# Kernel tuning notes

Hardware: AMD Instinct MI355X
Metric: run time of the kernel (lower is better)

The kernel has to match this reference:

```python
import jax, jax.numpy as jnp
import numpy as np

N = 2_000_000
NUM_IN = 9
F1, F2 = 32, 64
NUM_SEG = 100_000
EPS = 1e-5


def setup_inputs() -> dict:
    key = jax.random.key(0)
    ks = jax.random.split(key, 10)
    points = jax.random.normal(ks[0], (N, NUM_IN), dtype=jnp.float32)
    inverse_indices = jax.random.randint(ks[1], (N,), 0, NUM_SEG, dtype=jnp.int64)
    w1 = jax.random.normal(ks[2], (NUM_IN, F1), dtype=jnp.float32) / np.sqrt(NUM_IN)
    b1 = jax.random.normal(ks[3], (F1,), dtype=jnp.float32) * 0.01
    g1 = jnp.ones((F1,), jnp.float32)
    be1 = jnp.zeros((F1,), jnp.float32)
    w2 = jax.random.normal(ks[4], (F1, F2), dtype=jnp.float32) / np.sqrt(F1)
    b2 = jax.random.normal(ks[5], (F2,), dtype=jnp.float32) * 0.01
    g2 = jnp.ones((F2,), jnp.float32)
    be2 = jnp.zeros((F2,), jnp.float32)
    return {
        "points": points, "inverse_indices": inverse_indices, "num_segments": NUM_SEG,
        "w1": w1, "b1": b1, "g1": g1, "be1": be1,
        "w2": w2, "b2": b2, "g2": g2, "be2": be2,
    }


def _linear_bn_relu(x, w, b, gamma, beta):
    # Linear -> BatchNorm1d (training-mode batch stats, biased var, eps=1e-5) -> ReLU
    h = x @ w + b
    mean = h.mean(axis=0)
    var = h.var(axis=0)  # biased, matches torch BN normalization
    h = (h - mean) * jax.lax.rsqrt(var + EPS) * gamma + beta
    return jax.nn.relu(h)


def reference(points, inverse_indices, num_segments, w1, b1, g1, be1, w2, b2, g2, be2):
    feat = _linear_bn_relu(points, w1, b1, g1, be1)
    feat = _linear_bn_relu(feat, w2, b2, g2, be2)
    # scatter_max over dim 0; torch_scatter zero-initializes empty segments,
    # and post-ReLU features are >= 0, so clamp -inf (empty) to 0.
    seg = jax.ops.segment_max(feat, inverse_indices, num_segments=num_segments)
    return jnp.maximum(seg, 0.0)
```

## Files before the change

kernel.cpp:

```cpp
#include <hip/hip_runtime.h>

#define EPS 1e-5f
#define NIN 9
#define F1 32
#define F2 64
#define NMOM 45
#define ROWB 80
#define SHIFT 7
#define NSEGB 128
#define NBMAX 1024
#define BT_BIN 8192
#define WSTRIDE 68

#define WS_S    0
#define WS_M    16
#define WS_S2   64
#define WS_SS2  128
#define WS_SC1  192
#define WS_SH1  224
#define WS_W1P  256
#define WS_SC2  544
#define WS_SH2  608

typedef __attribute__((ext_vector_type(8))) short bf16x8;
typedef __attribute__((ext_vector_type(4))) float f32x4;

__device__ __forceinline__ unsigned int f2bf(float f) {
    unsigned int u = __float_as_uint(f);
    return (u + 0x7fffu + ((u >> 16) & 1u)) >> 16;
}
__device__ __forceinline__ unsigned int pack2(float lo, float hi) {
    return f2bf(lo) | (f2bf(hi) << 16);
}

__global__ __launch_bounds__(256, 4) void moments_kernel(
    const float* __restrict__ pts, const int* __restrict__ idx,
    float* __restrict__ ws, int* __restrict__ histc, int N, int nb)
{
    __shared__ int lhist[NBMAX];
    __shared__ float red[64];
    for (int t = threadIdx.x; t < nb; t += 256) lhist[t] = 0;

    float S[NIN], M[NMOM];
#pragma unroll
    for (int k = 0; k < NIN; ++k) S[k] = 0.f;
#pragma unroll
    for (int m = 0; m < NMOM; ++m) M[m] = 0.f;
    __syncthreads();

    const int stride = gridDim.x * blockDim.x;
    for (int i = blockIdx.x * blockDim.x + threadIdx.x; i < N; i += stride) {
        const float* p = pts + (size_t)i * NIN;
        atomicAdd(&lhist[idx[i] >> SHIFT], 1);
        float x[NIN];
#pragma unroll
        for (int k = 0; k < NIN; ++k) x[k] = p[k];
#pragma unroll
        for (int k = 0; k < NIN; ++k) {
            S[k] += x[k];
#pragma unroll
            for (int l = 0; l < NIN; ++l) {
                if (l >= k) {
                    const int m = k * NIN - (k * (k - 1)) / 2 + (l - k);
                    M[m] = fmaf(x[k], x[l], M[m]);
                }
            }
        }
    }
#pragma unroll
    for (int off = 32; off > 0; off >>= 1) {
#pragma unroll
        for (int k = 0; k < NIN; ++k) S[k] += __shfl_xor(S[k], off, 64);
#pragma unroll
        for (int m = 0; m < NMOM; ++m) M[m] += __shfl_xor(M[m], off, 64);
    }
    if (threadIdx.x < 64) red[threadIdx.x] = 0.f;
    __syncthreads();
    if ((threadIdx.x & 63) == 0) {
#pragma unroll
        for (int k = 0; k < NIN; ++k) atomicAdd(&red[WS_S + k], S[k]);
#pragma unroll
        for (int m = 0; m < NMOM; ++m) atomicAdd(&red[WS_M + m], M[m]);
    }
    __syncthreads();
    if (threadIdx.x < 64) atomicAdd(&ws[threadIdx.x], red[threadIdx.x]);
    for (int t = threadIdx.x; t < nb; t += 256)
        if (lhist[t] > 0) atomicAdd(&histc[t], lhist[t]);
}

__global__ void scan_coarse_kernel(const int* __restrict__ histc,
                                   int* __restrict__ offsets,
                                   int* __restrict__ cursor, int nb)
{
    __shared__ int part[256];
    const int tid = threadIdx.x;
    int v[4];
    int sum = 0;
    const int base = tid * 4;
#pragma unroll
    for (int j = 0; j < 4; ++j) {
        const int i = base + j;
        v[j] = (i < nb) ? histc[i] : 0;
        sum += v[j];
    }
    part[tid] = sum;
    __syncthreads();
    for (int d = 1; d < 256; d <<= 1) {
        int t = (tid >= d) ? part[tid - d] : 0;
        __syncthreads();
        part[tid] += t;
        __syncthreads();
    }
    int pre = part[tid] - sum;
#pragma unroll
    for (int j = 0; j < 4; ++j) {
        const int i = base + j;
        if (i < nb) { offsets[i] = pre; cursor[i] = pre; }
        pre += v[j];
    }
    if (tid == 255) offsets[nb] = part[255];
}

__global__ void finalize1_kernel(
    const float* __restrict__ w1, const float* __restrict__ b1,
    const float* __restrict__ g1, const float* __restrict__ be1,
    float* __restrict__ ws, float invN)
{
    __shared__ float sc1s[F1];
    const int j = threadIdx.x;
    if (j < F1) {
        float W[NIN];
        float P = 0.f;
#pragma unroll
        for (int k = 0; k < NIN; ++k) {
            W[k] = w1[k * F1 + j];
            P = fmaf(ws[WS_S + k], W[k], P);
        }
        float Q = 0.f;
        int m = 0;
#pragma unroll
        for (int k = 0; k < NIN; ++k) {
            Q = fmaf(ws[WS_M + m], W[k] * W[k], Q); ++m;
#pragma unroll
            for (int l = k + 1; l < NIN; ++l) {
                Q = fmaf(2.f * ws[WS_M + m], W[k] * W[l], Q); ++m;
            }
        }
        const float b = b1[j];
        const float mean = fmaf(P, invN, b);
        const float Eh2 = fmaf(fmaf(2.f * b, P, Q), invN, b * b);
        const float var = Eh2 - mean * mean;
        const float sc = g1[j] * rsqrtf(var + EPS);
        ws[WS_SC1 + j] = sc;
        ws[WS_SH1 + j] = be1[j] - mean * sc;
        sc1s[j] = sc;
    }
    __syncthreads();
    for (int m = threadIdx.x; m < NIN * F1; m += blockDim.x)
        ws[WS_W1P + m] = w1[m] * sc1s[m & (F1 - 1)];
}

__global__ void finalize2_kernel(
    const float* __restrict__ g2, const float* __restrict__ be2,
    const float* __restrict__ b2, float* __restrict__ ws, float invN, float padf)
{
    const int j = threadIdx.x;
    if (j < F2) {
        const float b = b2[j];
        const float S  = ws[WS_S2 + j]  - padf * b;
        const float SS = ws[WS_SS2 + j] - padf * b * b;
        const float mean = S * invN;
        const float var  = SS * invN - mean * mean;
        const float sc   = g2[j] * rsqrtf(var + EPS);
        ws[WS_SC2 + j] = sc;
        ws[WS_SH2 + j] = be2[j] - mean * sc;
    }
}

__device__ __forceinline__ void f1_row_bf16(
    const float* __restrict__ p, const float* __restrict__ wl,
    const float* __restrict__ sh1, unsigned int* __restrict__ pk )
{
    float x[NIN];
#pragma unroll
    for (int k = 0; k < NIN; ++k) x[k] = p[k];
#pragma unroll
    for (int fc = 0; fc < 4; ++fc) {
        float h[8];
#pragma unroll
        for (int jj = 0; jj < 8; ++jj) h[jj] = sh1[fc * 8 + jj];
#pragma unroll
        for (int k = 0; k < NIN; ++k) {
            const float xv = x[k];
#pragma unroll
            for (int jj = 0; jj < 8; ++jj)
                h[jj] = fmaf(xv, wl[k * F1 + fc * 8 + jj], h[jj]);
        }
#pragma unroll
        for (int jj = 0; jj < 4; ++jj)
            pk[fc * 4 + jj] = pack2(fmaxf(h[2 * jj], 0.f), fmaxf(h[2 * jj + 1], 0.f));
    }
}

__global__ __launch_bounds__(256, 3) void f1stats_kernel(
    const float* __restrict__ pts, const float* __restrict__ w2,
    const float* __restrict__ b2, float* __restrict__ ws,
    uint4* __restrict__ f1buf, int N)
{
    __shared__ __align__(16) unsigned char stag[4][64 * ROWB];
    __shared__ float red[2 * F2];

    const int lane = threadIdx.x & 63, wv = threadIdx.x >> 6;
    const int quad = lane >> 4, m16 = lane & 15;

    bf16x8 bfr[4];
#pragma unroll
    for (int nt = 0; nt < 4; ++nt)
#pragma unroll
        for (int j = 0; j < 8; ++j)
            bfr[nt][j] = (short)f2bf(w2[(quad * 8 + j) * F2 + nt * 16 + m16]);
    float b2f[4];
#pragma unroll
    for (int nt = 0; nt < 4; ++nt) b2f[nt] = b2[nt * 16 + m16];

    const float* wl  = ws + WS_W1P;
    const float* sh1 = ws + WS_SH1;
    const f32x4 zero = {0.f, 0.f, 0.f, 0.f};
    float s[4] = {0.f, 0.f, 0.f, 0.f}, ss[4] = {0.f, 0.f, 0.f, 0.f};

    unsigned char* myst = stag[wv];
    const int nchunks = (N + 63) / 64;
    for (int c = blockIdx.x * 4 + wv; c < nchunks; c += gridDim.x * 4) {
        const int i = c * 64 + lane;
        unsigned int pk[16];
        if (i < N) {
            f1_row_bf16(pts + (size_t)i * NIN, wl, sh1, pk);
        } else {
#pragma unroll
            for (int q = 0; q < 16; ++q) pk[q] = 0u;
        }
        uint4* wrow = (uint4*)(myst + lane * ROWB);
#pragma unroll
        for (int cidx = 0; cidx < 4; ++cidx)
            wrow[cidx] = make_uint4(pk[4*cidx+0], pk[4*cidx+1], pk[4*cidx+2], pk[4*cidx+3]);

        if (i < N) {
            uint4* dst = f1buf + (size_t)i * 4;
            dst[0] = make_uint4(pk[0],  pk[1],  pk[2],  pk[3]);
            dst[1] = make_uint4(pk[4],  pk[5],  pk[6],  pk[7]);
            dst[2] = make_uint4(pk[8],  pk[9],  pk[10], pk[11]);
            dst[3] = make_uint4(pk[12], pk[13], pk[14], pk[15]);
        }

        bf16x8 afr[4];
#pragma unroll
        for (int mt = 0; mt < 4; ++mt)
            afr[mt] = *(const bf16x8*)(myst + (mt * 16 + m16) * ROWB + quad * 16);
#pragma unroll
        for (int mt = 0; mt < 4; ++mt) {
#pragma unroll
            for (int nt = 0; nt < 4; ++nt) {
                f32x4 d = __builtin_amdgcn_mfma_f32_16x16x32_bf16(afr[mt], bfr[nt], zero, 0, 0, 0);
#pragma unroll
                for (int rr = 0; rr < 4; ++rr) {
                    const float v = d[rr] + b2f[nt];
                    s[nt] += v;
                    ss[nt] = fmaf(v, v, ss[nt]);
                }
            }
        }
    }

#pragma unroll
    for (int off = 16; off < 64; off <<= 1)
#pragma unroll
        for (int nt = 0; nt < 4; ++nt) {
            s[nt]  += __shfl_xor(s[nt], off, 64);
            ss[nt] += __shfl_xor(ss[nt], off, 64);
        }
    if (threadIdx.x < 2 * F2) red[threadIdx.x] = 0.f;
    __syncthreads();
    if (quad == 0) {
#pragma unroll
        for (int nt = 0; nt < 4; ++nt) {
            atomicAdd(&red[nt * 16 + m16], s[nt]);
            atomicAdd(&red[F2 + nt * 16 + m16], ss[nt]);
        }
    }
    __syncthreads();
    if (threadIdx.x < F2) {
        atomicAdd(&ws[WS_S2 + threadIdx.x],  red[threadIdx.x]);
        atomicAdd(&ws[WS_SS2 + threadIdx.x], red[F2 + threadIdx.x]);
    }
}

__global__ __launch_bounds__(256) void binning_kernel(
    const int* __restrict__ idx, int* __restrict__ cursor,
    int2* __restrict__ pair, int N, int nb)
{
    __shared__ int lcnt[NBMAX];
    __shared__ int runbase[NBMAX];
    const int tid = threadIdx.x;
    const int t0 = blockIdx.x * BT_BIN;
    for (int t = tid; t < nb; t += 256) lcnt[t] = 0;
    __syncthreads();
#pragma unroll 4
    for (int r = 0; r < BT_BIN / 256; ++r) {
        const int i = t0 + r * 256 + tid;
        if (i < N) atomicAdd(&lcnt[idx[i] >> SHIFT], 1);
    }
    __syncthreads();
    for (int t = tid; t < nb; t += 256) {
        const int c = lcnt[t];
        if (c > 0) runbase[t] = atomicAdd(&cursor[t], c);
        lcnt[t] = 0;
    }
    __syncthreads();
#pragma unroll 4
    for (int r = 0; r < BT_BIN / 256; ++r) {
        const int i = t0 + r * 256 + tid;
        if (i < N) {
            const int sg = idx[i];
            const int bb = sg >> SHIFT;
            const int p = runbase[bb] + atomicAdd(&lcnt[bb], 1);
            pair[p] = make_int2(i, sg);
        }
    }
}

__global__ __launch_bounds__(256, 3) void bucket_scatter_kernel(
    const uint4* __restrict__ f1buf, const int2* __restrict__ pair,
    const float* __restrict__ w2, const float* __restrict__ b2,
    const float* __restrict__ ws, const int* __restrict__ offsets,
    unsigned int* __restrict__ out, int nseg)
{
    __shared__ unsigned int win[NSEGB * WSTRIDE];
    __shared__ int2 prl[4][64];

    const int b = blockIdx.x;
    const int start = offsets[b], end = offsets[b + 1];
    const int tid = threadIdx.x;
    const int lane = tid & 63, wv = tid >> 6;
    const int quad = lane >> 4, m16 = lane & 15;

    for (int t = tid; t < NSEGB * WSTRIDE; t += 256) win[t] = 0u;

    bf16x8 bfr[4];
#pragma unroll
    for (int nt = 0; nt < 4; ++nt)
#pragma unroll
        for (int j = 0; j < 8; ++j)
            bfr[nt][j] = (short)f2bf(w2[(quad * 8 + j) * F2 + nt * 16 + m16]);
    float sc2f[4], shb[4];
#pragma unroll
    for (int nt = 0; nt < 4; ++nt) {
        const int f = nt * 16 + m16;
        sc2f[nt] = ws[WS_SC2 + f];
        shb[nt]  = fmaf(b2[f], sc2f[nt], ws[WS_SH2 + f]);
    }
    const f32x4 zero = {0.f, 0.f, 0.f, 0.f};
    __syncthreads();

    const int segbase = b << SHIFT;
    const int nch = (end - start + 63) >> 6;
    const bf16x8* fb = (const bf16x8*)f1buf;
    for (int c = wv; c < nch; c += 4) {
        const int cbase = start + c * 64;
        const int sp = cbase + lane;
        int2 pr = make_int2(0, -1);
        if (sp < end) {
            pr = pair[sp];
            pr.y -= segbase;
        }
        prl[wv][lane] = pr;

        bf16x8 afr[4];
#pragma unroll
        for (int mt = 0; mt < 4; ++mt) {
            if (cbase + mt * 16 + m16 < end) {
                const int gi = prl[wv][mt * 16 + m16].x;
                afr[mt] = fb[(size_t)gi * 4 + quad];
            } else {
#pragma unroll
                for (int j = 0; j < 8; ++j) afr[mt][j] = 0;
            }
        }
#pragma unroll
        for (int mt = 0; mt < 4; ++mt) {
            f32x4 d[4];
#pragma unroll
            for (int nt = 0; nt < 4; ++nt)
                d[nt] = __builtin_amdgcn_mfma_f32_16x16x32_bf16(afr[mt], bfr[nt], zero, 0, 0, 0);
#pragma unroll
            for (int rr = 0; rr < 4; ++rr) {
                const int sl = prl[wv][mt * 16 + quad * 4 + rr].y;
                if (sl >= 0) {
#pragma unroll
                    for (int nt = 0; nt < 4; ++nt) {
                        const float v = fmaf(d[nt][rr], sc2f[nt], shb[nt]);
                        if (v > 0.f)
                            atomicMax(&win[sl * WSTRIDE + nt * 16 + m16], __float_as_uint(v));
                    }
                }
            }
        }
    }
    __syncthreads();
    const int rows = min(NSEGB, nseg - segbase);
    for (int t = tid; t < rows * 64; t += 256)
        out[(size_t)(segbase + (t >> 6)) * 64 + (t & 63)] = win[(t >> 6) * WSTRIDE + (t & 63)];
}

__global__ __launch_bounds__(256, 3) void stats2_kernel(
    const float* __restrict__ pts, const float* __restrict__ w2,
    const float* __restrict__ b2, float* __restrict__ ws, int N)
{
    __shared__ __align__(16) unsigned char stag[4][64 * ROWB];
    __shared__ float red[2 * F2];

    const int lane = threadIdx.x & 63, wv = threadIdx.x >> 6;
    const int quad = lane >> 4, m16 = lane & 15;

    bf16x8 bfr[4];
#pragma unroll
    for (int nt = 0; nt < 4; ++nt)
#pragma unroll
        for (int j = 0; j < 8; ++j)
            bfr[nt][j] = (short)f2bf(w2[(quad * 8 + j) * F2 + nt * 16 + m16]);
    float b2f[4];
#pragma unroll
    for (int nt = 0; nt < 4; ++nt) b2f[nt] = b2[nt * 16 + m16];

    const float* wl  = ws + WS_W1P;
    const float* sh1 = ws + WS_SH1;
    const f32x4 zero = {0.f, 0.f, 0.f, 0.f};
    float s[4] = {0.f, 0.f, 0.f, 0.f}, ss[4] = {0.f, 0.f, 0.f, 0.f};

    unsigned char* myst = stag[wv];
    const int nchunks = (N + 63) / 64;
    for (int c = blockIdx.x * 4 + wv; c < nchunks; c += gridDim.x * 4) {
        const int i = c * 64 + lane;
        unsigned int pk[16];
        if (i < N) {
            f1_row_bf16(pts + (size_t)i * NIN, wl, sh1, pk);
        } else {
#pragma unroll
            for (int q = 0; q < 16; ++q) pk[q] = 0u;
        }
        uint4* wrow = (uint4*)(myst + lane * ROWB);
#pragma unroll
        for (int cidx = 0; cidx < 4; ++cidx)
            wrow[cidx] = make_uint4(pk[4*cidx+0], pk[4*cidx+1], pk[4*cidx+2], pk[4*cidx+3]);

        bf16x8 afr[4];
#pragma unroll
        for (int mt = 0; mt < 4; ++mt)
            afr[mt] = *(const bf16x8*)(myst + (mt * 16 + m16) * ROWB + quad * 16);
#pragma unroll
        for (int mt = 0; mt < 4; ++mt) {
#pragma unroll
            for (int nt = 0; nt < 4; ++nt) {
                f32x4 d = __builtin_amdgcn_mfma_f32_16x16x32_bf16(afr[mt], bfr[nt], zero, 0, 0, 0);
#pragma unroll
                for (int rr = 0; rr < 4; ++rr) {
                    const float v = d[rr] + b2f[nt];
                    s[nt] += v;
                    ss[nt] = fmaf(v, v, ss[nt]);
                }
            }
        }
    }
#pragma unroll
    for (int off = 16; off < 64; off <<= 1)
#pragma unroll
        for (int nt = 0; nt < 4; ++nt) {
            s[nt]  += __shfl_xor(s[nt], off, 64);
            ss[nt] += __shfl_xor(ss[nt], off, 64);
        }
    if (threadIdx.x < 2 * F2) red[threadIdx.x] = 0.f;
    __syncthreads();
    if (quad == 0) {
#pragma unroll
        for (int nt = 0; nt < 4; ++nt) {
            atomicAdd(&red[nt * 16 + m16], s[nt]);
            atomicAdd(&red[F2 + nt * 16 + m16], ss[nt]);
        }
    }
    __syncthreads();
    if (threadIdx.x < F2) {
        atomicAdd(&ws[WS_S2 + threadIdx.x],  red[threadIdx.x]);
        atomicAdd(&ws[WS_SS2 + threadIdx.x], red[F2 + threadIdx.x]);
    }
}

__global__ __launch_bounds__(256, 2) void bucket_scatter_gather_kernel(
    const float* __restrict__ pts, const int2* __restrict__ pair,
    const float* __restrict__ w2, const float* __restrict__ b2,
    const float* __restrict__ ws, const int* __restrict__ offsets,
    unsigned int* __restrict__ out, int nseg)
{
    __shared__ unsigned int win[NSEGB * WSTRIDE];
    __shared__ __align__(16) unsigned char stag[4][64 * ROWB];
    __shared__ int segl[4][64];

    const int b = blockIdx.x;
    const int start = offsets[b], end = offsets[b + 1];
    const int tid = threadIdx.x;
    const int lane = tid & 63, wv = tid >> 6;
    const int quad = lane >> 4, m16 = lane & 15;

    for (int t = tid; t < NSEGB * WSTRIDE; t += 256) win[t] = 0u;

    bf16x8 bfr[4];
#pragma unroll
    for (int nt = 0; nt < 4; ++nt)
#pragma unroll
        for (int j = 0; j < 8; ++j)
            bfr[nt][j] = (short)f2bf(w2[(quad * 8 + j) * F2 + nt * 16 + m16]);
    float sc2f[4], shb[4];
#pragma unroll
    for (int nt = 0; nt < 4; ++nt) {
        const int f = nt * 16 + m16;
        sc2f[nt] = ws[WS_SC2 + f];
        shb[nt]  = fmaf(b2[f], sc2f[nt], ws[WS_SH2 + f]);
    }
    const float* wl  = ws + WS_W1P;
    const float* sh1 = ws + WS_SH1;
    const f32x4 zero = {0.f, 0.f, 0.f, 0.f};
    __syncthreads();

    const int segbase = b << SHIFT;
    const int nch = (end - start + 63) >> 6;
    unsigned char* myst = stag[wv];
    for (int c = wv; c < nch; c += 4) {
        const int cbase = start + c * 64;
        const int sp = cbase + lane;
        unsigned int pk[16];
        int sl = -1;
        if (sp < end) {
            const int2 pr = pair[sp];
            f1_row_bf16(pts + (size_t)pr.x * NIN, wl, sh1, pk);
            sl = pr.y - segbase;
        } else {
#pragma unroll
            for (int q = 0; q < 16; ++q) pk[q] = 0u;
        }
        segl[wv][lane] = sl;
        uint4* wrow = (uint4*)(myst + lane * ROWB);
#pragma unroll
        for (int cidx = 0; cidx < 4; ++cidx)
            wrow[cidx] = make_uint4(pk[4*cidx+0], pk[4*cidx+1], pk[4*cidx+2], pk[4*cidx+3]);

        bf16x8 afr[4];
#pragma unroll
        for (int mt = 0; mt < 4; ++mt)
            afr[mt] = *(const bf16x8*)(myst + (mt * 16 + m16) * ROWB + quad * 16);
#pragma unroll
        for (int mt = 0; mt < 4; ++mt) {
            f32x4 d[4];
#pragma unroll
            for (int nt = 0; nt < 4; ++nt)
                d[nt] = __builtin_amdgcn_mfma_f32_16x16x32_bf16(afr[mt], bfr[nt], zero, 0, 0, 0);
#pragma unroll
            for (int rr = 0; rr < 4; ++rr) {
                const int sl2 = segl[wv][mt * 16 + quad * 4 + rr];
                if (sl2 >= 0) {
#pragma unroll
                    for (int nt = 0; nt < 4; ++nt) {
                        const float v = fmaf(d[nt][rr], sc2f[nt], shb[nt]);
                        if (v > 0.f)
                            atomicMax(&win[sl2 * WSTRIDE + nt * 16 + m16], __float_as_uint(v));
                    }
                }
            }
        }
    }
    __syncthreads();
    const int rows = min(NSEGB, nseg - segbase);
    for (int t = tid; t < rows * 64; t += 256)
        out[(size_t)(segbase + (t >> 6)) * 64 + (t & 63)] = win[(t >> 6) * WSTRIDE + (t & 63)];
}

extern "C" void kernel_launch(void* const* d_in, const int* in_sizes, int n_in,
                              void* d_out, int out_size, void* d_ws, size_t ws_size,
                              hipStream_t stream)
{
    const float* pts = (const float*)d_in[0];
    const int*   idx = (const int*)d_in[1];
    const float* w1  = (const float*)d_in[3];
    const float* b1  = (const float*)d_in[4];
    const float* g1  = (const float*)d_in[5];
    const float* be1 = (const float*)d_in[6];
    const float* w2  = (const float*)d_in[7];
    const float* b2  = (const float*)d_in[8];
    const float* g2  = (const float*)d_in[9];
    const float* be2 = (const float*)d_in[10];

    const int N = in_sizes[0] / NIN;
    const int nseg = out_size / F2;
    const int nb = (nseg + NSEGB - 1) >> SHIFT;
    const float invN = 1.0f / (float)N;
    const float padf = (float)((64 - (N & 63)) & 63);

    char* base = (char*)d_ws;
    const size_t f1bytes = (size_t)N * 64;
    const size_t pairbytes = (size_t)N * 8;
    const size_t tailbytes = 4096 + ((size_t)NBMAX + NBMAX + 1 + NBMAX) * sizeof(int) + 256;
    const size_t need_main = f1bytes + pairbytes + tailbytes;

    if (ws_size >= need_main) {
        uint4* f1buf   = (uint4*)base;
        int2*  pair    = (int2*)(base + f1bytes);
        float* ws      = (float*)(base + f1bytes + pairbytes);
        int*   histc   = (int*)(base + f1bytes + pairbytes + 4096);
        int*   offsets = histc + NBMAX;
        int*   cursor  = offsets + NBMAX + 1;

        hipMemsetAsync(ws, 0, 192 * sizeof(float), stream);
        hipMemsetAsync(histc, 0, NBMAX * sizeof(int), stream);

        moments_kernel<<<1024, 256, 0, stream>>>(pts, idx, ws, histc, N, nb);
        finalize1_kernel<<<1, 320, 0, stream>>>(w1, b1, g1, be1, ws, invN);
        scan_coarse_kernel<<<1, 256, 0, stream>>>(histc, offsets, cursor, nb);
        f1stats_kernel<<<1024, 256, 0, stream>>>(pts, w2, b2, ws, f1buf, N);
        binning_kernel<<<(N + BT_BIN - 1) / BT_BIN, 256, 0, stream>>>(
            idx, cursor, pair, N, nb);
        finalize2_kernel<<<1, 64, 0, stream>>>(g2, be2, b2, ws, invN, padf);
        bucket_scatter_kernel<<<nb, 256, 0, stream>>>(
            f1buf, pair, w2, b2, ws, offsets, (unsigned int*)d_out, nseg);
    } else {
        int2*  pair    = (int2*)base;
        float* ws      = (float*)(base + pairbytes);
        int*   histc   = (int*)(base + pairbytes + 4096);
        int*   offsets = histc + NBMAX;
        int*   cursor  = offsets + NBMAX + 1;

        hipMemsetAsync(ws, 0, 192 * sizeof(float), stream);
        hipMemsetAsync(histc, 0, NBMAX * sizeof(int), stream);

        moments_kernel<<<1024, 256, 0, stream>>>(pts, idx, ws, histc, N, nb);
        finalize1_kernel<<<1, 320, 0, stream>>>(w1, b1, g1, be1, ws, invN);
        scan_coarse_kernel<<<1, 256, 0, stream>>>(histc, offsets, cursor, nb);
        binning_kernel<<<(N + BT_BIN - 1) / BT_BIN, 256, 0, stream>>>(
            idx, cursor, pair, N, nb);
        stats2_kernel<<<1024, 256, 0, stream>>>(pts, w2, b2, ws, N);
        finalize2_kernel<<<1, 64, 0, stream>>>(g2, be2, b2, ws, invN, padf);
        bucket_scatter_gather_kernel<<<nb, 256, 0, stream>>>(
            pts, pair, w2, b2, ws, offsets, (unsigned int*)d_out, nseg);
    }
}
```

Measured before the change: 309.4 us.

## Write f1 features in binned order so the scatter pass reads contiguously

```diff
diff --git a/kernel.cpp b/kernel.cpp
--- a/kernel.cpp
+++ b/kernel.cpp
@@ -30,7 +30,9 @@
     return (u + 0x7fffu + ((u >> 16) & 1u)) >> 16;
 }
 __device__ __forceinline__ unsigned int pack2(float lo, float hi) {
-    return f2bf(lo) | (f2bf(hi) << 16);
+    unsigned int r;
+    asm("v_cvt_pk_bf16_f32 %0, %1, %2" : "=v"(r) : "v"(lo), "v"(hi));
+    return r;
 }
 
 __global__ __launch_bounds__(256, 4) void moments_kernel(
@@ -49,7 +51,29 @@
     __syncthreads();
 
     const int stride = gridDim.x * blockDim.x;
-    for (int i = blockIdx.x * blockDim.x + threadIdx.x; i < N; i += stride) {
+    int i = blockIdx.x * blockDim.x + threadIdx.x;
+    for (; i + stride < N; i += 2 * stride) {
+        const float* p0 = pts + (size_t)i * NIN;
+        const float* p1 = p0 + (size_t)stride * NIN;
+        atomicAdd(&lhist[idx[i] >> SHIFT], 1);
+        atomicAdd(&lhist[idx[i + stride] >> SHIFT], 1);
+        float x0[NIN], x1[NIN];
+#pragma unroll
+        for (int k = 0; k < NIN; ++k) { x0[k] = p0[k]; x1[k] = p1[k]; }
+#pragma unroll
+        for (int k = 0; k < NIN; ++k) {
+            S[k] += x0[k] + x1[k];
+#pragma unroll
+            for (int l = 0; l < NIN; ++l) {
+                if (l >= k) {
+                    const int m = k * NIN - (k * (k - 1)) / 2 + (l - k);
+                    M[m] = fmaf(x0[k], x0[l], M[m]);
+                    M[m] = fmaf(x1[k], x1[l], M[m]);
+                }
+            }
+        }
+    }
+    if (i < N) {
         const float* p = pts + (size_t)i * NIN;
         atomicAdd(&lhist[idx[i] >> SHIFT], 1);
         float x[NIN];
@@ -205,7 +229,7 @@
 __global__ __launch_bounds__(256, 3) void f1stats_kernel(
     const float* __restrict__ pts, const float* __restrict__ w2,
     const float* __restrict__ b2, float* __restrict__ ws,
-    uint4* __restrict__ f1buf, int N)
+    const int* __restrict__ posmap, uint4* __restrict__ f1buf, int N)
 {
     __shared__ __align__(16) unsigned char stag[4][64 * ROWB];
     __shared__ float red[2 * F2];
@@ -245,7 +269,8 @@
             wrow[cidx] = make_uint4(pk[4*cidx+0], pk[4*cidx+1], pk[4*cidx+2], pk[4*cidx+3]);
 
         if (i < N) {
-            uint4* dst = f1buf + (size_t)i * 4;
+            const int p = posmap[i];
+            uint4* dst = f1buf + (size_t)p * 4;
             dst[0] = make_uint4(pk[0],  pk[1],  pk[2],  pk[3]);
             dst[1] = make_uint4(pk[4],  pk[5],  pk[6],  pk[7]);
             dst[2] = make_uint4(pk[8],  pk[9],  pk[10], pk[11]);
@@ -294,7 +319,42 @@
     }
 }
 
-__global__ __launch_bounds__(256) void binning_kernel(
+__global__ __launch_bounds__(256) void binning_seg_kernel(
+    const int* __restrict__ idx, int* __restrict__ cursor,
+    int* __restrict__ segs, int* __restrict__ posmap, int N, int nb)
+{
+    __shared__ int lcnt[NBMAX];
+    __shared__ int runbase[NBMAX];
+    const int tid = threadIdx.x;
+    const int t0 = blockIdx.x * BT_BIN;
+    for (int t = tid; t < nb; t += 256) lcnt[t] = 0;
+    __syncthreads();
+#pragma unroll 4
+    for (int r = 0; r < BT_BIN / 256; ++r) {
+        const int i = t0 + r * 256 + tid;
+        if (i < N) atomicAdd(&lcnt[idx[i] >> SHIFT], 1);
+    }
+    __syncthreads();
+    for (int t = tid; t < nb; t += 256) {
+        const int c = lcnt[t];
+        if (c > 0) runbase[t] = atomicAdd(&cursor[t], c);
+        lcnt[t] = 0;
+    }
+    __syncthreads();
+#pragma unroll 4
+    for (int r = 0; r < BT_BIN / 256; ++r) {
+        const int i = t0 + r * 256 + tid;
+        if (i < N) {
+            const int sg = idx[i];
+            const int bb = sg >> SHIFT;
+            const int p = runbase[bb] + atomicAdd(&lcnt[bb], 1);
+            segs[p] = sg;
+            posmap[i] = p;
+        }
+    }
+}
+
+__global__ __launch_bounds__(256) void binning_pair_kernel(
     const int* __restrict__ idx, int* __restrict__ cursor,
     int2* __restrict__ pair, int N, int nb)
 {
@@ -329,13 +389,14 @@
 }
 
 __global__ __launch_bounds__(256, 3) void bucket_scatter_kernel(
-    const uint4* __restrict__ f1buf, const int2* __restrict__ pair,
+    const uint4* __restrict__ f1buf, const int* __restrict__ segs,
     const float* __restrict__ w2, const float* __restrict__ b2,
+    const float* __restrict__ g2, const float* __restrict__ be2,
     const float* __restrict__ ws, const int* __restrict__ offsets,
-    unsigned int* __restrict__ out, int nseg)
+    unsigned int* __restrict__ out, int nseg, float invN, float padf)
 {
     __shared__ unsigned int win[NSEGB * WSTRIDE];
-    __shared__ int2 prl[4][64];
+    __shared__ int segl[4][64];
 
     const int b = blockIdx.x;
     const int start = offsets[b], end = offsets[b + 1];
@@ -355,8 +416,14 @@
 #pragma unroll
     for (int nt = 0; nt < 4; ++nt) {
         const int f = nt * 16 + m16;
-        sc2f[nt] = ws[WS_SC2 + f];
-        shb[nt]  = fmaf(b2[f], sc2f[nt], ws[WS_SH2 + f]);
+        const float bb2 = b2[f];
+        const float Sv  = ws[WS_S2 + f]  - padf * bb2;
+        const float SSv = ws[WS_SS2 + f] - padf * bb2 * bb2;
+        const float mean = Sv * invN;
+        const float var  = SSv * invN - mean * mean;
+        const float sc   = g2[f] * rsqrtf(var + EPS);
+        sc2f[nt] = sc;
+        shb[nt]  = fmaf(bb2, sc, be2[f] - mean * sc);
     }
     const f32x4 zero = {0.f, 0.f, 0.f, 0.f};
     __syncthreads();
@@ -367,19 +434,16 @@
     for (int c = wv; c < nch; c += 4) {
         const int cbase = start + c * 64;
         const int sp = cbase + lane;
-        int2 pr = make_int2(0, -1);
-        if (sp < end) {
-            pr = pair[sp];
-            pr.y -= segbase;
-        }
-        prl[wv][lane] = pr;
+        int sl = -1;
+        if (sp < end) sl = segs[sp] - segbase;
+        segl[wv][lane] = sl;
 
         bf16x8 afr[4];
 #pragma unroll
         for (int mt = 0; mt < 4; ++mt) {
-            if (cbase + mt * 16 + m16 < end) {
-                const int gi = prl[wv][mt * 16 + m16].x;
-                afr[mt] = fb[(size_t)gi * 4 + quad];
+            const int row = cbase + mt * 16 + m16;
+            if (row < end) {
+                afr[mt] = fb[(size_t)row * 4 + quad];
             } else {
 #pragma unroll
                 for (int j = 0; j < 8; ++j) afr[mt][j] = 0;
@@ -393,13 +457,13 @@
                 d[nt] = __builtin_amdgcn_mfma_f32_16x16x32_bf16(afr[mt], bfr[nt], zero, 0, 0, 0);
 #pragma unroll
             for (int rr = 0; rr < 4; ++rr) {
-                const int sl = prl[wv][mt * 16 + quad * 4 + rr].y;
-                if (sl >= 0) {
+                const int sl2 = segl[wv][mt * 16 + quad * 4 + rr];
+                if (sl2 >= 0) {
 #pragma unroll
                     for (int nt = 0; nt < 4; ++nt) {
                         const float v = fmaf(d[nt][rr], sc2f[nt], shb[nt]);
                         if (v > 0.f)
-                            atomicMax(&win[sl * WSTRIDE + nt * 16 + m16], __float_as_uint(v));
+                            atomicMax(&win[sl2 * WSTRIDE + nt * 16 + m16], __float_as_uint(v));
                     }
                 }
             }
@@ -608,9 +672,15 @@
     const size_t tailbytes = 4096 + ((size_t)NBMAX + NBMAX + 1 + NBMAX) * sizeof(int) + 256;
     const size_t need_main = f1bytes + pairbytes + tailbytes;
 
+    const int nch = (N + 63) / 64;
+    int f1grid = (nch + 3) / 4;
+    if (f1grid > 1792) f1grid = 1792;
+    if (f1grid < 1) f1grid = 1;
+
     if (ws_size >= need_main) {
         uint4* f1buf   = (uint4*)base;
-        int2*  pair    = (int2*)(base + f1bytes);
+        int*   segs    = (int*)(base + f1bytes);
+        int*   posmap  = (int*)(base + f1bytes + (size_t)N * 4);
         float* ws      = (float*)(base + f1bytes + pairbytes);
         int*   histc   = (int*)(base + f1bytes + pairbytes + 4096);
         int*   offsets = histc + NBMAX;
@@ -622,12 +692,12 @@
         moments_kernel<<<1024, 256, 0, stream>>>(pts, idx, ws, histc, N, nb);
         finalize1_kernel<<<1, 320, 0, stream>>>(w1, b1, g1, be1, ws, invN);
         scan_coarse_kernel<<<1, 256, 0, stream>>>(histc, offsets, cursor, nb);
-        f1stats_kernel<<<1024, 256, 0, stream>>>(pts, w2, b2, ws, f1buf, N);
-        binning_kernel<<<(N + BT_BIN - 1) / BT_BIN, 256, 0, stream>>>(
-            idx, cursor, pair, N, nb);
-        finalize2_kernel<<<1, 64, 0, stream>>>(g2, be2, b2, ws, invN, padf);
+        binning_seg_kernel<<<(N + BT_BIN - 1) / BT_BIN, 256, 0, stream>>>(
+            idx, cursor, segs, posmap, N, nb);
+        f1stats_kernel<<<f1grid, 256, 0, stream>>>(pts, w2, b2, ws, posmap, f1buf, N);
         bucket_scatter_kernel<<<nb, 256, 0, stream>>>(
-            f1buf, pair, w2, b2, ws, offsets, (unsigned int*)d_out, nseg);
+            f1buf, segs, w2, b2, g2, be2, ws, offsets, (unsigned int*)d_out,
+            nseg, invN, padf);
     } else {
         int2*  pair    = (int2*)base;
         float* ws      = (float*)(base + pairbytes);
@@ -641,7 +711,7 @@
         moments_kernel<<<1024, 256, 0, stream>>>(pts, idx, ws, histc, N, nb);
         finalize1_kernel<<<1, 320, 0, stream>>>(w1, b1, g1, be1, ws, invN);
         scan_coarse_kernel<<<1, 256, 0, stream>>>(histc, offsets, cursor, nb);
-        binning_kernel<<<(N + BT_BIN - 1) / BT_BIN, 256, 0, stream>>>(
+        binning_pair_kernel<<<(N + BT_BIN - 1) / BT_BIN, 256, 0, stream>>>(
             idx, cursor, pair, N, nb);
         stats2_kernel<<<1024, 256, 0, stream>>>(pts, w2, b2, ws, N);
         finalize2_kernel<<<1, 64, 0, stream>>>(g2, be2, b2, ws, invN, padf);
```

New measurement: 320.7 us. +3.7%, slower.
